# Optimization experiments

Measured on AMD Instinct MI355X. Metric: run time of the kernel, lower is better.

## Reference

```python
import jax, jax.numpy as jnp
import numpy as np

M = 2048  # pooled grid rows (init arg m)
N = 2048  # pooled grid cols (init arg n); code requires m == n


def setup_inputs() -> dict:
    key = jax.random.key(0)
    d_coarse = jax.random.normal(key, (2 * M, 2 * N), dtype=jnp.float32)
    return {"d_coarse": d_coarse}


def reference(d_coarse):
    m, n = M, N
    # MaxPool2d(kernel_size=2, stride=2) on the (2m, 2n) coarse depth map -> (m, n)
    d_pool = d_coarse.reshape(m, 2, n, 2).max(axis=(1, 3))

    k_noise, k_drop = jax.random.split(jax.random.key(1))
    # Noise module: torch.rand_like * stdev(1) + mean(0)  (uniform [0,1) noise)
    noise = jax.random.uniform(k_noise, d_pool.shape, dtype=d_pool.dtype)
    d_noised = d_pool + noise

    # IntervalThreshold: (max - min) / min(m, n)
    thr = (jnp.max(d_pool) - jnp.min(d_pool)) / min(m, n)

    rows = jnp.arange(m)[:, None]  # i index
    cols = jnp.arange(n)[None, :]  # j index
    adj = jnp.zeros((m, n), dtype=bool)

    # ReconGraph: only diagonal offsets survive (dx != 0 and dy != 0),
    # i.e. (dx, dy) in {-1, 1}^2. For each (i, j) compare d[i+dy, j+dx] vs d[i, j].
    for dx in (-1, 1):
        for dy in (-1, 1):
            # shifted[i, j] == d_noised[i + dy, j + dx]
            shifted = jnp.roll(d_noised, shift=(-dy, -dx), axis=(0, 1))
            ok = jnp.abs(shifted - d_noised) <= thr
            # Original boundary conditions, plus in-range guards on the
            # actually-accessed indices (i+dy, j+dx).
            mask = ((rows + dx >= 0) & (rows + dy < m)
                    & (cols + dx >= 0) & (cols + dy < n)
                    & (rows + dy >= 0) & (cols + dx < n))
            # Write goes to adjacency_matrix[j, i] -> transpose (m == n).
            adj = adj | (ok & mask).T

    # GraphDropout with p=0.5: bernoulli keep mask on the boolean matrix
    # (self.train is the bound method -> truthy, so dropout always applies).
    keep = jax.random.bernoulli(k_drop, 0.5, adj.shape)
    return adj & keep
```

## Files before the change

### kernel.cpp

```cpp
#include <hip/hip_runtime.h>

typedef unsigned int u32;

#define HALF_T 2097152u
#define NPX 2048
#define NPOOL_BLOCKS 4096

__host__ __device__ inline void tf2x32(u32 k0, u32 k1, u32& x0, u32& x1) {
  const u32 ks2 = k0 ^ k1 ^ 0x1BD11BDAu;
  x0 += k0; x1 += k1;
#define TFR(r) { x0 += x1; x1 = (x1 << (r)) | (x1 >> (32 - (r))); x1 ^= x0; }
  TFR(13) TFR(15) TFR(26) TFR(6)
  x0 += k1;  x1 += ks2 + 1u;
  TFR(17) TFR(29) TFR(16) TFR(24)
  x0 += ks2; x1 += k0 + 2u;
  TFR(13) TFR(15) TFR(26) TFR(6)
  x0 += k0;  x1 += k1 + 3u;
  TFR(17) TFR(29) TFR(16) TFR(24)
  x0 += k1;  x1 += ks2 + 4u;
  TFR(13) TFR(15) TFR(26) TFR(6)
  x0 += ks2; x1 += k0 + 5u;
#undef TFR
}

__device__ inline u32 pbits(u32 k0, u32 k1, u32 t) {
  u32 x0 = 0u, x1 = t;
  tf2x32(k0, k1, x0, x1);
  return x0 ^ x1;
}

__device__ inline float bits_to_uniform(u32 bits) {
  return __uint_as_float((bits >> 9) | 0x3F800000u) - 1.0f;
}

__global__ __launch_bounds__(256) void k_pool_nostore(const float* __restrict__ coarse,
                                                      float* __restrict__ pmin,
                                                      float* __restrict__ pmax) {
  const u32 g = blockIdx.x * 256 + threadIdx.x;
  const int i  = g >> 10;
  const int jj = g & 1023;
  const float4* r0 = (const float4*)(coarse + (size_t)(2*i       ) * 4096);
  const float4* r1 = (const float4*)(coarse + (size_t)(2*i + 1   ) * 4096);
  const float4* r2 = (const float4*)(coarse + (size_t)(2*i + 2048) * 4096);
  const float4* r3 = (const float4*)(coarse + (size_t)(2*i + 2049) * 4096);
  const float4 a = r0[jj], b = r1[jj], c = r2[jj], d = r3[jj];

  const float p0a = fmaxf(fmaxf(a.x, a.y), fmaxf(b.x, b.y));
  const float p0b = fmaxf(fmaxf(a.z, a.w), fmaxf(b.z, b.w));
  const float p1a = fmaxf(fmaxf(c.x, c.y), fmaxf(d.x, d.y));
  const float p1b = fmaxf(fmaxf(c.z, c.w), fmaxf(d.z, d.w));

  float lmin = fminf(fminf(p0a, p0b), fminf(p1a, p1b));
  float lmax = fmaxf(fmaxf(p0a, p0b), fmaxf(p1a, p1b));

  for (int off = 32; off > 0; off >>= 1) {
    lmin = fminf(lmin, __shfl_down(lmin, off, 64));
    lmax = fmaxf(lmax, __shfl_down(lmax, off, 64));
  }
  __shared__ float smin[4], smax[4];
  const int lane = threadIdx.x & 63, wv = threadIdx.x >> 6;
  if (lane == 0) { smin[wv] = lmin; smax[wv] = lmax; }
  __syncthreads();
  if (threadIdx.x == 0) {
    pmin[blockIdx.x] = fminf(fminf(smin[0], smin[1]), fminf(smin[2], smin[3]));
    pmax[blockIdx.x] = fmaxf(fmaxf(smax[0], smax[1]), fmaxf(smax[2], smax[3]));
  }
}

__device__ inline float block_thr(const float* __restrict__ pmin,
                                  const float* __restrict__ pmax,
                                  int tid) {
  __shared__ float smin[16], smax[16], sthr;
  float lmin = INFINITY, lmax = -INFINITY;
#pragma unroll
  for (int k = 0; k < NPOOL_BLOCKS; k += 1024) {
    lmin = fminf(lmin, pmin[tid + k]);
    lmax = fmaxf(lmax, pmax[tid + k]);
  }
  for (int off = 32; off > 0; off >>= 1) {
    lmin = fminf(lmin, __shfl_down(lmin, off, 64));
    lmax = fmaxf(lmax, __shfl_down(lmax, off, 64));
  }
  const int lane = tid & 63, wv = tid >> 6;
  if (lane == 0) { smin[wv] = lmin; smax[wv] = lmax; }
  __syncthreads();
  if (tid == 0) {
    float gmin = smin[0], gmax = smax[0];
#pragma unroll
    for (int w = 1; w < 16; ++w) {
      gmin = fminf(gmin, smin[w]);
      gmax = fmaxf(gmax, smax[w]);
    }
    sthr = (gmax - gmin) / 2048.0f;
  }
  __syncthreads();
  return sthr;
}

__device__ inline bool adj_eval(const float s[34][35], int tx, int ty,
                                int c, int rr, float thr) {
  const float ctr = s[tx+1][ty+1];
  const bool cge1 = (c  >= 1),    cle = (c  <= NPX - 2);
  const bool rge1 = (rr >= 1),    rle = (rr <= NPX - 2);
  bool a = false;
  if (cge1 && rge1)                    a |= (fabsf(s[tx  ][ty  ] - ctr) <= thr);
  if (cge1 && cle && rge1 && rle)      a |= (fabsf(s[tx+2][ty  ] - ctr) <= thr);
  if (cge1 && rle)                     a |= (fabsf(s[tx  ][ty+2] - ctr) <= thr);
  if (cle  && rle)                     a |= (fabsf(s[tx+2][ty+2] - ctr) <= thr);
  return a;
}

__device__ inline float dn_compute(const float* __restrict__ coarse,
                                   int i, int j, u32 kn0, u32 kn1) {
  const float2* r0 = (const float2*)(coarse + (size_t)(2*i    ) * 4096);
  const float2* r1 = (const float2*)(coarse + (size_t)(2*i + 1) * 4096);
  float2 a = r0[j], b = r1[j];
  float p = fmaxf(fmaxf(a.x, a.y), fmaxf(b.x, b.y));
  return p + bits_to_uniform(pbits(kn0, kn1, (u32)(i * NPX + j)));
}

__global__ __launch_bounds__(1024) void k_graph_fused(const float* __restrict__ coarse,
                                                      const float* __restrict__ pmin,
                                                      const float* __restrict__ pmax,
                                                      int* __restrict__ out,
                                                      u32 kn0, u32 kn1, u32 kd0, u32 kd1) {
  __shared__ float s0[34][35];
  __shared__ float s1[34][35];
  const int tid = threadIdx.y * 32 + threadIdx.x;
  const float thr = block_thr(pmin, pmax, tid);
  const int c0 = blockIdx.x * 32, r0 = blockIdx.y * 32;
  for (int idx = tid; idx < 34 * 34; idx += 1024) {
    const int lc = idx / 34, lr = idx - lc * 34;
    const int c = c0 - 1 + lc;
    const int r = r0 - 1 + lr;
    float v0 = 0.f, v1 = 0.f;
    if ((unsigned)c < (unsigned)NPX) {
      if ((unsigned)r < (unsigned)NPX)      v0 = dn_compute(coarse, c, r, kn0, kn1);
      const int r2 = r + 1024;
      if ((unsigned)r2 < (unsigned)NPX)     v1 = dn_compute(coarse, c, r2, kn0, kn1);
    }
    s0[lc][lr] = v0;
    s1[lc][lr] = v1;
  }
  __syncthreads();
  const int tx = threadIdx.x, ty = threadIdx.y;
  const int c = c0 + tx, r = r0 + ty;
  const bool adj0 = adj_eval(s0, tx, ty, c, r,        thr);
  const bool adj1 = adj_eval(s1, tx, ty, c, r + 1024, thr);
  const u32 t0 = (u32)(r * NPX + c);
  const bool keep0 = !(pbits(kd0, kd1, t0)          >> 31);
  const bool keep1 = !(pbits(kd0, kd1, t0 + HALF_T) >> 31);
  out[(size_t)r * NPX + c]          = (adj0 && keep0) ? 1 : 0;
  out[(size_t)(r + 1024) * NPX + c] = (adj1 && keep1) ? 1 : 0;
}

extern "C" void kernel_launch(void* const* d_in, const int* in_sizes, int n_in,
                              void* d_out, int out_size, void* d_ws, size_t ws_size,
                              hipStream_t stream) {
  const float* coarse = (const float*)d_in[0];
  int* out = (int*)d_out;

  u32 a0 = 0u, a1 = 0u; tf2x32(0u, 1u, a0, a1);
  u32 b0 = 0u, b1 = 1u; tf2x32(0u, 1u, b0, b1);
  const u32 kn0 = a0, kn1 = a1, kd0 = b0, kd1 = b1;

  char* ws = (char*)d_ws;
  float* pmin = (float*)ws;
  float* pmax = (float*)(ws + 16384);

  k_pool_nostore<<<NPOOL_BLOCKS, 256, 0, stream>>>(coarse, pmin, pmax);
  k_graph_fused<<<dim3(64, 32), dim3(32, 32), 0, stream>>>(coarse, pmin, pmax, out,
                                                           kn0, kn1, kd0, kd1);
}
```

Before: 125.9 us.

## Materialize noised pooled map in first kernel instead of recomputing in graph kernel

The pooling kernel now also adds threefry noise and writes the noised pooled map (16 MB) to workspace, and the graph kernel reads that map instead of reloading coarse data and recomputing pooling plus noise for each halo tile. Before this, the coarse input was read twice and the PRNG was evaluated redundantly for halo cells. The trade is an extra 16 MB write and read of the intermediate, in exchange for removing the second 64 MB coarse pass and the redundant hash work.

```diff
diff --git a/kernel.cpp b/kernel.cpp
--- a/kernel.cpp
+++ b/kernel.cpp
@@ -33,25 +33,35 @@
   return __uint_as_float((bits >> 9) | 0x3F800000u) - 1.0f;
 }
 
-__global__ __launch_bounds__(256) void k_pool_nostore(const float* __restrict__ coarse,
-                                                      float* __restrict__ pmin,
-                                                      float* __restrict__ pmax) {
+__global__ __launch_bounds__(256) void k_pool(const float* __restrict__ coarse,
+                                              float4* __restrict__ dn4,
+                                              float* __restrict__ pmin,
+                                              float* __restrict__ pmax,
+                                              u32 kn0, u32 kn1) {
   const u32 g = blockIdx.x * 256 + threadIdx.x;
-  const int i  = g >> 10;
-  const int jj = g & 1023;
-  const float4* r0 = (const float4*)(coarse + (size_t)(2*i       ) * 4096);
-  const float4* r1 = (const float4*)(coarse + (size_t)(2*i + 1   ) * 4096);
-  const float4* r2 = (const float4*)(coarse + (size_t)(2*i + 2048) * 4096);
-  const float4* r3 = (const float4*)(coarse + (size_t)(2*i + 2049) * 4096);
-  const float4 a = r0[jj], b = r1[jj], c = r2[jj], d = r3[jj];
+  const int i  = g >> 9;
+  const int jj = g & 511;
 
-  const float p0a = fmaxf(fmaxf(a.x, a.y), fmaxf(b.x, b.y));
-  const float p0b = fmaxf(fmaxf(a.z, a.w), fmaxf(b.z, b.w));
-  const float p1a = fmaxf(fmaxf(c.x, c.y), fmaxf(d.x, d.y));
-  const float p1b = fmaxf(fmaxf(c.z, c.w), fmaxf(d.z, d.w));
+  const float4* r0 = (const float4*)(coarse + (size_t)(2*i    ) * 4096);
+  const float4* r1 = (const float4*)(coarse + (size_t)(2*i + 1) * 4096);
+  const float4 a0 = r0[2*jj], a1 = r0[2*jj + 1];
+  const float4 b0 = r1[2*jj], b1 = r1[2*jj + 1];
 
-  float lmin = fminf(fminf(p0a, p0b), fminf(p1a, p1b));
-  float lmax = fmaxf(fmaxf(p0a, p0b), fmaxf(p1a, p1b));
+  const float p0 = fmaxf(fmaxf(a0.x, a0.y), fmaxf(b0.x, b0.y));
+  const float p1 = fmaxf(fmaxf(a0.z, a0.w), fmaxf(b0.z, b0.w));
+  const float p2 = fmaxf(fmaxf(a1.x, a1.y), fmaxf(b1.x, b1.y));
+  const float p3 = fmaxf(fmaxf(a1.z, a1.w), fmaxf(b1.z, b1.w));
+
+  float lmin = fminf(fminf(p0, p1), fminf(p2, p3));
+  float lmax = fmaxf(fmaxf(p0, p1), fmaxf(p2, p3));
+
+  const u32 t0 = (u32)i * 2048u + 4u * (u32)jj;
+  float4 o;
+  o.x = p0 + bits_to_uniform(pbits(kn0, kn1, t0));
+  o.y = p1 + bits_to_uniform(pbits(kn0, kn1, t0 + 1u));
+  o.z = p2 + bits_to_uniform(pbits(kn0, kn1, t0 + 2u));
+  o.w = p3 + bits_to_uniform(pbits(kn0, kn1, t0 + 3u));
+  dn4[g] = o;
 
   for (int off = 32; off > 0; off >>= 1) {
     lmin = fminf(lmin, __shfl_down(lmin, off, 64));
@@ -110,24 +120,16 @@
   return a;
 }
 
-__device__ inline float dn_compute(const float* __restrict__ coarse,
-                                   int i, int j, u32 kn0, u32 kn1) {
-  const float2* r0 = (const float2*)(coarse + (size_t)(2*i    ) * 4096);
-  const float2* r1 = (const float2*)(coarse + (size_t)(2*i + 1) * 4096);
-  float2 a = r0[j], b = r1[j];
-  float p = fmaxf(fmaxf(a.x, a.y), fmaxf(b.x, b.y));
-  return p + bits_to_uniform(pbits(kn0, kn1, (u32)(i * NPX + j)));
-}
-
-__global__ __launch_bounds__(1024) void k_graph_fused(const float* __restrict__ coarse,
-                                                      const float* __restrict__ pmin,
-                                                      const float* __restrict__ pmax,
-                                                      int* __restrict__ out,
-                                                      u32 kn0, u32 kn1, u32 kd0, u32 kd1) {
+__global__ __launch_bounds__(1024) void k_graph(const float* __restrict__ dn,
+                                                const float* __restrict__ pmin,
+                                                const float* __restrict__ pmax,
+                                                int* __restrict__ out,
+                                                u32 kd0, u32 kd1) {
   __shared__ float s0[34][35];
   __shared__ float s1[34][35];
   const int tid = threadIdx.y * 32 + threadIdx.x;
   const float thr = block_thr(pmin, pmax, tid);
+
   const int c0 = blockIdx.x * 32, r0 = blockIdx.y * 32;
   for (int idx = tid; idx < 34 * 34; idx += 1024) {
     const int lc = idx / 34, lr = idx - lc * 34;
@@ -135,9 +137,9 @@
     const int r = r0 - 1 + lr;
     float v0 = 0.f, v1 = 0.f;
     if ((unsigned)c < (unsigned)NPX) {
-      if ((unsigned)r < (unsigned)NPX)      v0 = dn_compute(coarse, c, r, kn0, kn1);
+      if ((unsigned)r < (unsigned)NPX)          v0 = dn[c * NPX + r];
       const int r2 = r + 1024;
-      if ((unsigned)r2 < (unsigned)NPX)     v1 = dn_compute(coarse, c, r2, kn0, kn1);
+      if ((unsigned)r2 < (unsigned)NPX)         v1 = dn[c * NPX + r2];
     }
     s0[lc][lr] = v0;
     s1[lc][lr] = v1;
@@ -167,8 +169,8 @@
   char* ws = (char*)d_ws;
   float* pmin = (float*)ws;
   float* pmax = (float*)(ws + 16384);
+  float* dn   = (float*)(ws + 32768);
 
-  k_pool_nostore<<<NPOOL_BLOCKS, 256, 0, stream>>>(coarse, pmin, pmax);
-  k_graph_fused<<<dim3(64, 32), dim3(32, 32), 0, stream>>>(coarse, pmin, pmax, out,
-                                                           kn0, kn1, kd0, kd1);
+  k_pool<<<NPOOL_BLOCKS, 256, 0, stream>>>(coarse, (float4*)dn, pmin, pmax, kn0, kn1);
+  k_graph<<<dim3(64, 32), dim3(32, 32), 0, stream>>>(dn, pmin, pmax, out, kd0, kd1);
 }
```

After: 118.0 us. 1.07x faster.
